# Kernel optimization log

Hardware: AMD Instinct MI355X
Metric: run time of the kernel (lower is better)

## Reference

```python
import jax, jax.numpy as jnp
import numpy as np

DIM = 768
NUM_HEADS = 12
HEAD_DIM = DIM // NUM_HEADS
SCALE = HEAD_DIM ** -0.5


def setup_inputs() -> dict:
    key = jax.random.key(0)
    ks = jax.random.split(key, 12)
    B, N, C, H = 8, 1024, DIM, NUM_HEADS
    s = 0.02
    return {
        'q_in': jax.random.normal(ks[0], (B, N, C), jnp.float32),
        'kv_in': jax.random.normal(ks[1], (B, N, C), jnp.float32),
        'Wq': jax.random.normal(ks[2], (C, C), jnp.float32) * s,
        'Wk': jax.random.normal(ks[3], (C, C), jnp.float32) * s,
        'Wv': jax.random.normal(ks[4], (C, C), jnp.float32) * s,
        'Wp': jax.random.normal(ks[5], (C, C), jnp.float32) * s,
        'bp': jnp.zeros((C,), jnp.float32),
        'W_dy2': jax.random.normal(ks[6], (H, C), jnp.float32) * s,  # lf gate linear (out=H)
        'b_dy2': jnp.zeros((H,), jnp.float32),
        'W_dy': jax.random.normal(ks[7], (H, C), jnp.float32) * s,   # hf gate linear
        'b_dy': jnp.zeros((H,), jnp.float32),
        'lf_gamma': jnp.full((C,), 1e-5, jnp.float32),
        'hf_gamma': jnp.full((C,), 1e-5, jnp.float32),
        'star_scale': jnp.ones((1,), jnp.float32),
        'star_bias': jnp.zeros((1,), jnp.float32),
    }


def reference(q_in, kv_in, Wq, Wk, Wv, Wp, bp, W_dy2, b_dy2, W_dy, b_dy,
              lf_gamma, hf_gamma, star_scale, star_bias):
    B, Nq, C = q_in.shape
    Nk = kv_in.shape[1]
    H, D = NUM_HEADS, HEAD_DIM

    # StarReLU on query tokens (ignore_cls_token = 0)
    dy_feat = star_scale * jnp.square(jax.nn.relu(q_in)) + star_bias  # (B,Nq,C)

    # low-freq dynamic gate: tanh(linear) per head, repeated over head_dim
    dy_lf = jnp.tanh(jnp.einsum('bnc,hc->bnh', dy_feat, W_dy2) + b_dy2)  # (B,Nq,H)
    dy_lf = jnp.repeat(dy_lf, D, axis=-1)  # (B,Nq,C)

    # high-freq dynamic gate: rational-of-softplus^2
    dy = jax.nn.softplus(jnp.einsum('bnc,hc->bnh', dy_feat, W_dy) + b_dy)
    dy2 = jnp.square(dy)
    dy_hf = 2.0 * dy2 / (dy2 + 0.3678)
    dy_hf = jnp.repeat(dy_hf, D, axis=-1)  # (B,Nq,C)

    # projections (torch Linear: y = x @ W.T), split heads
    q = jnp.einsum('bnc,dc->bnd', q_in, Wq).reshape(B, Nq, H, D).transpose(0, 2, 1, 3)
    k = jnp.einsum('bnc,dc->bnd', kv_in, Wk).reshape(B, Nk, H, D).transpose(0, 2, 1, 3)
    v = jnp.einsum('bnc,dc->bnd', kv_in, Wv).reshape(B, Nk, H, D).transpose(0, 2, 1, 3)

    attn = jnp.einsum('bhqd,bhkd->bhqk', q * SCALE, k)
    attn = jax.nn.softmax(attn, axis=-1)
    x_attn = jnp.einsum('bhqk,bhkd->bhqd', attn, v)
    x_attn = x_attn.transpose(0, 2, 1, 3).reshape(B, Nq, C)

    # Nk == Nq branch: per-token residual high-frequency component
    v_reshape = v.transpose(0, 2, 1, 3).reshape(B, Nk, C)
    v_hf = v_reshape - x_attn

    x_attn = x_attn + x_attn * dy_lf * lf_gamma
    x_attn = x_attn + dy_hf * v_hf * hf_gamma

    out = jnp.einsum('bnc,dc->bnd', x_attn, Wp) + bp
    return out
```

## Files before the change

kernel.cpp:

```cpp
#include <hip/hip_runtime.h>
#include <hip/hip_bf16.h>
#include <stdint.h>

typedef unsigned short u16;
typedef unsigned int u32;
typedef unsigned long long u64;
typedef __attribute__((ext_vector_type(8))) short short8;
typedef __attribute__((ext_vector_type(4))) float f32x4;

#define LOG2E 1.44269504f

static __device__ __forceinline__ u16 f2bf(float f) {
    u32 x = __float_as_uint(f);
    u32 r = (x + 0x7FFFu + ((x >> 16) & 1u)) >> 16;
    return (u16)r;
}
static __device__ __forceinline__ float bf2f(u16 u) {
    return __uint_as_float(((u32)u) << 16);
}
static __device__ __forceinline__ u32 pk2(float lo, float hi) {
    __hip_bfloat162 t = __float22bfloat162_rn(float2{lo, hi});
    union { __hip_bfloat162 b; u32 u; } cv;
    cv.b = t;
    return cv.u;
}

static __device__ __forceinline__ void g2l16(const void* g, void* l) {
    __builtin_amdgcn_global_load_lds((const __attribute__((address_space(1))) void*)g,
                                     (__attribute__((address_space(3))) void*)l, 16, 0, 0);
}

__global__ __launch_bounds__(256) void k_cvt_all(
    const float* __restrict__ q_in, const float* __restrict__ kv_in,
    const float* __restrict__ Wq, const float* __restrict__ Wk,
    const float* __restrict__ Wv, const float* __restrict__ Wp,
    const float* __restrict__ Wdy2, const float* __restrict__ Wdy,
    u16* __restrict__ qbf, u16* __restrict__ kvbf, u16* __restrict__ Wqb,
    u16* __restrict__ Wkb, u16* __restrict__ Wvb, u16* __restrict__ Wpb,
    u16* __restrict__ wgb) {
    int i = blockIdx.x * 256 + threadIdx.x;
    const float* src;
    u16* dst;
    int so, dofs;
    if (i < 786432) { src = q_in; dst = qbf; so = i; dofs = i; }
    else if (i < 1572864) { src = kv_in; dst = kvbf; so = i - 786432; dofs = so; }
    else if (i < 1646592) { src = Wq; dst = Wqb; so = i - 1572864; dofs = so; }
    else if (i < 1720320) { src = Wk; dst = Wkb; so = i - 1646592; dofs = so; }
    else if (i < 1794048) { src = Wv; dst = Wvb; so = i - 1720320; dofs = so; }
    else if (i < 1867776) { src = Wp; dst = Wpb; so = i - 1794048; dofs = so; }
    else if (i < 1870080) {
        int e = i - 1867776;
        dst = wgb; dofs = e;
        if (e < 1152) { src = Wdy2; so = e; }
        else { src = Wdy; so = e - 1152; }
    } else return;
    const float4* p = (const float4*)src + (size_t)so * 2;
    float4 a = p[0], b = p[1];
    short8 o;
    o[0] = f2bf(a.x); o[1] = f2bf(a.y); o[2] = f2bf(a.z); o[3] = f2bf(a.w);
    o[4] = f2bf(b.x); o[5] = f2bf(b.y); o[6] = f2bf(b.z); o[7] = f2bf(b.w);
    *((short8*)dst + dofs) = o;
}

__global__ __launch_bounds__(64) void k_gates(
    const u16* __restrict__ qbf, const u16* __restrict__ wgb,
    const float* __restrict__ bdy2, const float* __restrict__ bdy,
    const float* __restrict__ star_s, const float* __restrict__ star_b,
    float* __restrict__ glf, float* __restrict__ ghf) {
    int lane = threadIdx.x;
    int g = lane >> 4, c = lane & 15;
    int row0 = blockIdx.x * 16;
    float ss = star_s[0], sb = star_b[0];
    f32x4 acc[2];
    acc[0] = (f32x4){0.f, 0.f, 0.f, 0.f};
    acc[1] = (f32x4){0.f, 0.f, 0.f, 0.f};
    for (int t = 0; t < 24; ++t) {
        int k0 = t * 32;
        short8 x8 = *(const short8*)(qbf + (size_t)(row0 + c) * 768 + k0 + g * 8);
        float f[8];
#pragma unroll
        for (int j = 0; j < 8; ++j) {
            float x = fmaxf(bf2f((u16)x8[j]), 0.f);
            f[j] = ss * x * x + sb;
        }
        union { u32 u[4]; short8 s8; } au;
#pragma unroll
        for (int j = 0; j < 4; ++j) au.u[j] = pk2(f[2 * j], f[2 * j + 1]);
        short8 b0 = *(const short8*)(wgb + (size_t)c * 768 + k0 + g * 8);
        short8 b1 = (short8){0, 0, 0, 0, 0, 0, 0, 0};
        if (c < 8)
            b1 = *(const short8*)(wgb + (size_t)(16 + c) * 768 + k0 + g * 8);
        acc[0] = __builtin_amdgcn_mfma_f32_16x16x32_bf16(au.s8, b0, acc[0], 0, 0, 0);
        acc[1] = __builtin_amdgcn_mfma_f32_16x16x32_bf16(au.s8, b1, acc[1], 0, 0, 0);
    }
#pragma unroll
    for (int n = 0; n < 2; ++n)
#pragma unroll
        for (int r = 0; r < 4; ++r) {
            int token = row0 + g * 4 + r;
            int o = n * 16 + c;
            float v = acc[n][r];
            if (o < 12) {
                glf[(size_t)token * 12 + o] = tanhf(v + bdy2[o]);
            } else if (o < 24) {
                float x = v + bdy[o - 12];
                float sp = (x > 15.f) ? x : log1pf(expf(x));
                float d2 = sp * sp;
                ghf[(size_t)token * 12 + (o - 12)] = 2.f * d2 / (d2 + 0.3678f);
            }
        }
}

__device__ __forceinline__ void gemm_core(const u16* __restrict__ A,
                                          const u16* __restrict__ W, u16* As,
                                          u16* Bs, int rowA0, int rowB0,
                                          int lane, int w, int wm, int wn,
                                          f32x4 acc[4][4]) {
    int g = lane >> 4, c = lane & 15;
#pragma unroll
    for (int m = 0; m < 4; ++m)
#pragma unroll
        for (int n = 0; n < 4; ++n) acc[m][n] = (f32x4){0.f, 0.f, 0.f, 0.f};

    auto stage = [&](int buf, int k0) {
#pragma unroll
        for (int j = 0; j < 2; ++j) {
            int idx = w * 128 + j * 64 + lane;
            int row = idx >> 2;
            int sl = (idx & 3) ^ (row & 3);
            size_t goA = (size_t)(rowA0 + row) * 768 + k0 + sl * 8;
            size_t goB = (size_t)(rowB0 + row) * 768 + k0 + sl * 8;
            int lo = (w * 128 + j * 64) * 8;
            g2l16(A + goA, As + buf * 4096 + lo);
            g2l16(W + goB, Bs + buf * 4096 + lo);
        }
    };

    stage(0, 0);
    __syncthreads();
    int buf = 0;
    for (int t = 0; t < 24; ++t) {
        if (t < 23) stage(buf ^ 1, (t + 1) * 32);
        short8 a[4], b[4];
#pragma unroll
        for (int m = 0; m < 4; ++m)
            a[m] = *(const short8*)(As + buf * 4096 +
                                    (wm * 64 + m * 16 + c) * 32 +
                                    (g ^ (c & 3)) * 8);
#pragma unroll
        for (int n = 0; n < 4; ++n)
            b[n] = *(const short8*)(Bs + buf * 4096 +
                                    (wn * 64 + n * 16 + c) * 32 +
                                    (g ^ (c & 3)) * 8);
#pragma unroll
        for (int m = 0; m < 4; ++m)
#pragma unroll
            for (int n = 0; n < 4; ++n)
                acc[m][n] = __builtin_amdgcn_mfma_f32_16x16x32_bf16(
                    a[m], b[n], acc[m][n], 0, 0, 0);
        __syncthreads();
        buf ^= 1;
    }
}

__global__ __launch_bounds__(256, 2) void k_gemm_qkv(
    const u16* __restrict__ qbf, const u16* __restrict__ kvbf,
    const u16* __restrict__ Wqb, const u16* __restrict__ Wkb,
    const u16* __restrict__ Wvb, u16* __restrict__ Qb, u16* __restrict__ Kb,
    u16* __restrict__ VTg, u16* __restrict__ vlin) {
    __shared__ __align__(16) u16 smem[16384];
    u16* As = smem;
    u16* Bs = smem + 8192;
    int bid = blockIdx.x;
    int logical = (bid & 7) * 144 + (bid >> 3);
    int panel = logical / 18, sub = logical % 18;
    int type = sub / 6, tn = sub % 6;
    int tid = threadIdx.x, lane = tid & 63, w = tid >> 6;
    int g = lane >> 4, c = lane & 15;
    int wm = w >> 1, wn = w & 1;
    int rowA0 = panel * 128, rowB0 = tn * 128;
    const u16* A = (type == 0) ? qbf : kvbf;
    const u16* W = (type == 0) ? Wqb : (type == 1) ? Wkb : Wvb;

    f32x4 acc[4][4];
    gemm_core(A, W, As, Bs, rowA0, rowB0, lane, w, wm, wn, acc);

    if (type == 0) {
        const float scl = 0.125f * LOG2E;
#pragma unroll
        for (int m = 0; m < 4; ++m)
#pragma unroll
            for (int n = 0; n < 4; ++n)
#pragma unroll
                for (int r = 0; r < 4; ++r) {
                    int row = rowA0 + wm * 64 + m * 16 + g * 4 + r;
                    int col = rowB0 + wn * 64 + n * 16 + c;
                    int bb = row >> 10, nn = row & 1023, hh = col >> 6,
                        dd = col & 63;
                    Qb[((size_t)(bb * 12 + hh) << 16) + (nn << 6) + dd] =
                        f2bf(acc[m][n][r] * scl);
                }
    } else if (type == 1) {
#pragma unroll
        for (int m = 0; m < 4; ++m)
#pragma unroll
            for (int n = 0; n < 4; ++n)
#pragma unroll
                for (int r = 0; r < 4; ++r) {
                    int row = rowA0 + wm * 64 + m * 16 + g * 4 + r;
                    int col = rowB0 + wn * 64 + n * 16 + c;
                    int bb = row >> 10, nn = row & 1023, hh = col >> 6,
                        dd = col & 63;
                    Kb[((size_t)(bb * 12 + hh) << 16) + (nn << 6) + dd] =
                        f2bf(acc[m][n][r]);
                }
    } else {
#pragma unroll
        for (int m = 0; m < 4; ++m)
#pragma unroll
            for (int n = 0; n < 4; ++n)
#pragma unroll
                for (int r = 0; r < 4; ++r) {
                    int row = rowA0 + wm * 64 + m * 16 + g * 4 + r;
                    int col = rowB0 + wn * 64 + n * 16 + c;
                    vlin[(size_t)row * 768 + col] = f2bf(acc[m][n][r]);
                }
        __syncthreads();
#pragma unroll
        for (int m = 0; m < 4; ++m)
#pragma unroll
            for (int n = 0; n < 4; ++n)
#pragma unroll
                for (int r = 0; r < 4; ++r) {
                    int rl = wm * 64 + m * 16 + g * 4 + r;
                    int cl = wn * 64 + n * 16 + c;
                    smem[cl * 128 + rl] = f2bf(acc[m][n][r]);
                }
        __syncthreads();
        int bb = rowA0 >> 10, nn0 = rowA0 & 1023;
#pragma unroll
        for (int j = 0; j < 8; ++j) {
            int idx = j * 256 + tid;
            int rT = idx >> 4, cc = idx & 15;
            int dout = rowB0 + rT, hh = dout >> 6, dd = dout & 63;
            const u16* srow = smem + rT * 128 + cc * 8;
            size_t robase = ((size_t)(bb * 12 + hh) * 64 + dd) * 1024;
#pragma unroll
            for (int e2 = 0; e2 < 4; ++e2) {
                int n0 = nn0 + cc * 8 + 2 * e2;
                int t6 = n0 & 63;
                int pos = (((t6 >> 1) & 1) << 5) | (((t6 >> 2) & 3) << 3) |
                          (((t6 >> 4) & 3) << 1) | (t6 & 1);
                u32 val = (u32)srow[2 * e2] | ((u32)srow[2 * e2 + 1] << 16);
                *(u32*)(VTg + robase + (n0 & ~63) + pos) = val;
            }
        }
    }
}

__global__ __launch_bounds__(256, 2) void k_gemm_out(
    const u16* __restrict__ xf, const u16* __restrict__ Wpb,
    const float* __restrict__ bp, float* __restrict__ out) {
    __shared__ __align__(16) u16 smem[16384];
    u16* As = smem;
    u16* Bs = smem + 8192;
    int bid = blockIdx.x;
    int logical = (bid & 7) * 48 + (bid >> 3);
    int c48 = logical % 48;
    int tm = (logical / 48) * 8 + c48 / 6, tn = c48 % 6;
    int tid = threadIdx.x, lane = tid & 63, w = tid >> 6;
    int wm = w >> 1, wn = w & 1;
    int rowA0 = tm * 128, rowB0 = tn * 128;

    f32x4 acc[4][4];
    gemm_core(xf, Wpb, As, Bs, rowA0, rowB0, lane, w, wm, wn, acc);

#pragma unroll
    for (int m = 0; m < 4; ++m)
#pragma unroll
        for (int n = 0; n < 4; ++n)
#pragma unroll
            for (int r = 0; r < 4; ++r) {
                int row = rowA0 + wm * 64 + m * 16 + (lane >> 4) * 4 + r;
                int col = rowB0 + wn * 64 + n * 16 + (lane & 15);
                out[(size_t)row * 768 + col] = acc[m][n][r] + bp[col];
            }
}

__global__ __launch_bounds__(256, 2) void k_attn(
    const u16* __restrict__ Qb, const u16* __restrict__ Kb,
    const u16* __restrict__ VTg, const u16* __restrict__ vlin,
    const float* __restrict__ glf, const float* __restrict__ ghf,
    const float* __restrict__ lfg, const float* __restrict__ hfg,
    u16* __restrict__ xfinal) {
    __shared__ __align__(16) u16 Ks[2][4096];
    __shared__ __align__(16) u16 Vs[2][4096];
    int b8 = blockIdx.x;
    int sw = (b8 & 7) * 96 + (b8 >> 3);
    int bh = sw >> 3, qblk = sw & 7;
    int bb = bh / 12, hh = bh % 12;
    int tid = threadIdx.x, lane = tid & 63, w = tid >> 6;
    int g = lane >> 4, c = lane & 15;
    const char* Kp = (const char*)(Kb + ((size_t)bh << 16));
    const char* Vp = (const char*)(VTg + ((size_t)bh << 16));
    const u16* Qp = Qb + ((size_t)bh << 16);
    int q0 = qblk * 128 + w * 32;

    short8 qf[2][2];
#pragma unroll
    for (int qb = 0; qb < 2; ++qb)
#pragma unroll
        for (int ks = 0; ks < 2; ++ks)
            qf[qb][ks] = *(const short8*)(Qp + (size_t)(q0 + qb * 16 + c) * 64 +
                                          ks * 32 + g * 8);

    f32x4 o[2][4];
#pragma unroll
    for (int qb = 0; qb < 2; ++qb)
#pragma unroll
        for (int n = 0; n < 4; ++n) o[qb][n] = (f32x4){0.f, 0.f, 0.f, 0.f};
    float lsum[2] = {0.f, 0.f};

    int kgo[2], vgo[2], ldo[2];
#pragma unroll
    for (int h = 0; h < 2; ++h) {
        int idx = w * 64 + lane + h * 256;
        int row = idx >> 3;
        int colb = ((idx & 7) * 16) ^ ((row & 7) << 4);
        kgo[h] = row * 128 + colb;
        vgo[h] = row * 2048 + colb;
        ldo[h] = (w * 64 + h * 256) * 16;
    }

    auto stage = [&](int bi, int t) {
#pragma unroll
        for (int h = 0; h < 2; ++h) {
            g2l16(Kp + (size_t)t * 8192 + kgo[h], (char*)&Ks[bi][0] + ldo[h]);
            g2l16(Vp + (size_t)t * 128 + vgo[h], (char*)&Vs[bi][0] + ldo[h]);
        }
    };

    stage(0, 0);
    __syncthreads();
    int buf = 0;
    int cs = (c & 7) << 4;
    for (int t = 0; t < 16; ++t) {
        if (t < 15) stage(buf ^ 1, t + 1);
        const char* Kbase = (const char*)&Ks[buf][0];
        const char* Vbase = (const char*)&Vs[buf][0];
        short8 kf[4][2], vf[4][2];
#pragma unroll
        for (int m = 0; m < 4; ++m) {
            int rowb = (m * 16 + c) * 128;
#pragma unroll
            for (int ks = 0; ks < 2; ++ks)
                kf[m][ks] = *(const short8*)(Kbase + rowb +
                                             ((g * 16 + ks * 64) ^ cs));
        }
#pragma unroll
        for (int n = 0; n < 4; ++n) {
            int rowb = (n * 16 + c) * 128;
#pragma unroll
            for (int a = 0; a < 2; ++a)
                vf[n][a] = *(const short8*)(Vbase + rowb +
                                            ((a * 64 + g * 16) ^ cs));
        }
#pragma unroll
        for (int qb = 0; qb < 2; ++qb) {
            f32x4 s[4];
            __builtin_amdgcn_s_setprio(1);
#pragma unroll
            for (int m = 0; m < 4; ++m) {
                s[m] = __builtin_amdgcn_mfma_f32_16x16x32_bf16(
                    kf[m][0], qf[qb][0], (f32x4){0.f, 0.f, 0.f, 0.f}, 0, 0, 0);
                s[m] = __builtin_amdgcn_mfma_f32_16x16x32_bf16(
                    kf[m][1], qf[qb][1], s[m], 0, 0, 0);
            }
            __builtin_amdgcn_s_setprio(0);
            u32 P2[4][2];
            float ls = 0.f;
#pragma unroll
            for (int m = 0; m < 4; ++m) {
#pragma unroll
                for (int r = 0; r < 4; ++r) {
                    s[m][r] = exp2f(s[m][r]);
                    ls += s[m][r];
                }
                P2[m][0] = pk2(s[m][0], s[m][1]);
                P2[m][1] = pk2(s[m][2], s[m][3]);
            }
            lsum[qb] += ls;
#pragma unroll
            for (int a = 0; a < 2; ++a) {
                union { u32 u[4]; short8 s8; } pu;
                pu.u[0] = P2[0][a]; pu.u[1] = P2[1][a];
                pu.u[2] = P2[2][a]; pu.u[3] = P2[3][a];
                __builtin_amdgcn_s_setprio(1);
#pragma unroll
                for (int n = 0; n < 4; ++n)
                    o[qb][n] = __builtin_amdgcn_mfma_f32_16x16x32_bf16(
                        pu.s8, vf[n][a], o[qb][n], 0, 0, 0);
                __builtin_amdgcn_s_setprio(0);
            }
        }
        __syncthreads();
        buf ^= 1;
    }

#pragma unroll
    for (int qb = 0; qb < 2; ++qb) {
        float L = lsum[qb];
        L += __shfl_xor(L, 16);
        L += __shfl_xor(L, 32);
        float rl[4], alf[4], ahf[4];
        size_t trow[4];
#pragma unroll
        for (int r = 0; r < 4; ++r) {
            rl[r] = 1.0f / __shfl(L, g * 4 + r);
            int q = q0 + qb * 16 + 4 * g + r;
            trow[r] = (size_t)(bb * 1024 + q);
            alf[r] = glf[trow[r] * 12 + hh];
            ahf[r] = ghf[trow[r] * 12 + hh];
        }
#pragma unroll
        for (int n = 0; n < 4; ++n) {
            int col = hh * 64 + n * 16 + c;
            float lf = lfg[col], hf = hfg[col];
#pragma unroll
            for (int r = 0; r < 4; ++r) {
                float xa = o[qb][n][r] * rl[r];
                float v = bf2f(vlin[trow[r] * 768 + col]);
                float val = xa + xa * alf[r] * lf + ahf[r] * (v - xa) * hf;
                xfinal[trow[r] * 768 + col] = f2bf(val);
            }
        }
    }
}

extern "C" void kernel_launch(void* const* d_in, const int* in_sizes, int n_in,
                              void* d_out, int out_size, void* d_ws,
                              size_t ws_size, hipStream_t stream) {
    const float* q_in = (const float*)d_in[0];
    const float* kv_in = (const float*)d_in[1];
    const float* Wq = (const float*)d_in[2];
    const float* Wk = (const float*)d_in[3];
    const float* Wv = (const float*)d_in[4];
    const float* Wp = (const float*)d_in[5];
    const float* bp = (const float*)d_in[6];
    const float* Wdy2 = (const float*)d_in[7];
    const float* bdy2 = (const float*)d_in[8];
    const float* Wdy = (const float*)d_in[9];
    const float* bdy = (const float*)d_in[10];
    const float* lfg = (const float*)d_in[11];
    const float* hfg = (const float*)d_in[12];
    const float* st_s = (const float*)d_in[13];
    const float* st_b = (const float*)d_in[14];
    float* out = (float*)d_out;

    char* ws = (char*)d_ws;
    const size_t MC2 = (size_t)8192 * 768 * 2;
    const size_t WB = (size_t)768 * 768 * 2;
    u16* qbf = (u16*)(ws);
    u16* kvbf = (u16*)(ws + MC2);
    u16* Wqb = (u16*)(ws + 2 * MC2);
    u16* Wkb = (u16*)(ws + 2 * MC2 + WB);
    u16* Wvb = (u16*)(ws + 2 * MC2 + 2 * WB);
    u16* Wpb = (u16*)(ws + 2 * MC2 + 3 * WB);
    u16* Qb = (u16*)(ws + 2 * MC2 + 4 * WB);
    u16* Kb = (u16*)(ws + 3 * MC2 + 4 * WB);
    u16* VTg = (u16*)(ws + 4 * MC2 + 4 * WB);
    u16* vlin = (u16*)(ws + 5 * MC2 + 4 * WB);
    float* glf = (float*)(ws + 6 * MC2 + 4 * WB);
    float* ghf = (float*)(ws + 6 * MC2 + 4 * WB + (size_t)8192 * 12 * 4);
    u16* wgb = (u16*)(ws + 6 * MC2 + 4 * WB + (size_t)8192 * 12 * 8);
    u16* xfinal = qbf;

    k_cvt_all<<<7305, 256, 0, stream>>>(q_in, kv_in, Wq, Wk, Wv, Wp, Wdy2,
                                        Wdy, qbf, kvbf, Wqb, Wkb, Wvb, Wpb,
                                        wgb);
    k_gates<<<512, 64, 0, stream>>>(qbf, wgb, bdy2, bdy, st_s, st_b, glf, ghf);
    k_gemm_qkv<<<1152, 256, 0, stream>>>(qbf, kvbf, Wqb, Wkb, Wvb, Qb, Kb,
                                         VTg, vlin);
    k_attn<<<768, 256, 0, stream>>>(Qb, Kb, VTg, vlin, glf, ghf, lfg, hfg,
                                    xfinal);
    k_gemm_out<<<384, 256, 0, stream>>>(xfinal, Wpb, bp, out);
}
```

Measured before the change: 157.6 us.

## Change GEMM LDS swizzle to row-pair layout and stage attention epilogue through LDS

Result: no change. 159.1 us (+0.9%).

```diff
diff --git a/kernel.cpp b/kernel.cpp
--- a/kernel.cpp
+++ b/kernel.cpp
@@ -125,14 +125,14 @@
     auto stage = [&](int buf, int k0) {
 #pragma unroll
         for (int j = 0; j < 2; ++j) {
-            int idx = w * 128 + j * 64 + lane;
-            int row = idx >> 2;
-            int sl = (idx & 3) ^ (row & 3);
-            size_t goA = (size_t)(rowA0 + row) * 768 + k0 + sl * 8;
-            size_t goB = (size_t)(rowB0 + row) * 768 + k0 + sl * 8;
-            int lo = (w * 128 + j * 64) * 8;
-            g2l16(A + goA, As + buf * 4096 + lo);
-            g2l16(W + goB, Bs + buf * 4096 + lo);
+            int L = w * 128 + j * 64 + lane;
+            int p = L >> 3, s8 = L & 7;
+            int t2 = s8 ^ (p & 7);
+            int row = 2 * p + (t2 >> 2);
+            int chunk = t2 & 3;
+            size_t go = (size_t)row * 768 + k0 + chunk * 8;
+            g2l16(A + (size_t)rowA0 * 768 + go, As + buf * 4096 + L * 8);
+            g2l16(W + (size_t)rowB0 * 768 + go, Bs + buf * 4096 + L * 8);
         }
     };
 
@@ -143,15 +143,19 @@
         if (t < 23) stage(buf ^ 1, (t + 1) * 32);
         short8 a[4], b[4];
 #pragma unroll
-        for (int m = 0; m < 4; ++m)
-            a[m] = *(const short8*)(As + buf * 4096 +
-                                    (wm * 64 + m * 16 + c) * 32 +
-                                    (g ^ (c & 3)) * 8);
-#pragma unroll
-        for (int n = 0; n < 4; ++n)
-            b[n] = *(const short8*)(Bs + buf * 4096 +
-                                    (wn * 64 + n * 16 + c) * 32 +
-                                    (g ^ (c & 3)) * 8);
+        for (int m = 0; m < 4; ++m) {
+            int row = wm * 64 + m * 16 + c;
+            int off = (row >> 1) * 64 +
+                      ((((row & 1) << 2) | g) ^ ((row >> 1) & 7)) * 8;
+            a[m] = *(const short8*)(As + buf * 4096 + off);
+        }
+#pragma unroll
+        for (int n = 0; n < 4; ++n) {
+            int row = wn * 64 + n * 16 + c;
+            int off = (row >> 1) * 64 +
+                      ((((row & 1) << 2) | g) ^ ((row >> 1) & 7)) * 8;
+            b[n] = *(const short8*)(Bs + buf * 4096 + off);
+        }
 #pragma unroll
         for (int m = 0; m < 4; ++m)
 #pragma unroll
@@ -407,32 +411,54 @@
         buf ^= 1;
     }
 
+    u16* X = &Ks[0][0];
 #pragma unroll
     for (int qb = 0; qb < 2; ++qb) {
         float L = lsum[qb];
         L += __shfl_xor(L, 16);
         L += __shfl_xor(L, 32);
-        float rl[4], alf[4], ahf[4];
-        size_t trow[4];
-#pragma unroll
-        for (int r = 0; r < 4; ++r) {
-            rl[r] = 1.0f / __shfl(L, g * 4 + r);
-            int q = q0 + qb * 16 + 4 * g + r;
-            trow[r] = (size_t)(bb * 1024 + q);
-            alf[r] = glf[trow[r] * 12 + hh];
-            ahf[r] = ghf[trow[r] * 12 + hh];
-        }
-#pragma unroll
-        for (int n = 0; n < 4; ++n) {
-            int col = hh * 64 + n * 16 + c;
-            float lf = lfg[col], hf = hfg[col];
+        float rl[4];
+#pragma unroll
+        for (int r = 0; r < 4; ++r) rl[r] = 1.0f / __shfl(L, g * 4 + r);
+#pragma unroll
+        for (int n = 0; n < 4; ++n)
 #pragma unroll
             for (int r = 0; r < 4; ++r) {
-                float xa = o[qb][n][r] * rl[r];
-                float v = bf2f(vlin[trow[r] * 768 + col]);
-                float val = xa + xa * alf[r] * lf + ahf[r] * (v - xa) * hf;
-                xfinal[trow[r] * 768 + col] = f2bf(val);
-            }
+                int row = w * 32 + qb * 16 + 4 * g + r;
+                int col = n * 16 + c;
+                int byte = row * 128 + ((col * 2) ^ ((row & 3) << 4));
+                *(u16*)((char*)X + byte) = f2bf(o[qb][n][r] * rl[r]);
+            }
+    }
+    __syncthreads();
+    {
+        int row = tid >> 1, half = tid & 1;
+        size_t token = (size_t)bb * 1024 + qblk * 128 + row;
+        float alf = glf[token * 12 + hh];
+        float ahf = ghf[token * 12 + hh];
+        int dbase = hh * 64 + half * 32;
+        const u16* vbase = vlin + token * 768 + dbase;
+        u16* obase = xfinal + token * 768 + dbase;
+#pragma unroll
+        for (int j = 0; j < 4; ++j) {
+            int phys = ((half * 4 + j) ^ (row & 3)) * 16;
+            short8 xa8 = *(const short8*)((char*)X + row * 128 + phys);
+            short8 vl8 = *(const short8*)(vbase + j * 8);
+            float4 lg0 = *(const float4*)(lfg + dbase + j * 8);
+            float4 lg1 = *(const float4*)(lfg + dbase + j * 8 + 4);
+            float4 hg0 = *(const float4*)(hfg + dbase + j * 8);
+            float4 hg1 = *(const float4*)(hfg + dbase + j * 8 + 4);
+            float lg[8] = {lg0.x, lg0.y, lg0.z, lg0.w, lg1.x, lg1.y, lg1.z, lg1.w};
+            float hg[8] = {hg0.x, hg0.y, hg0.z, hg0.w, hg1.x, hg1.y, hg1.z, hg1.w};
+            short8 oo;
+#pragma unroll
+            for (int e = 0; e < 8; ++e) {
+                float xa = bf2f((u16)xa8[e]);
+                float v = bf2f((u16)vl8[e]);
+                float val = xa + xa * alf * lg[e] + ahf * (v - xa) * hg[e];
+                oo[e] = f2bf(val);
+            }
+            *(short8*)(obase + j * 8) = oo;
         }
     }
 }
```
